# Optimization experiments

Measured on AMD Instinct MI355X. Metric: run time of the kernel, lower is better.

## Reference

```python
import jax, jax.numpy as jnp
import numpy as np
import math

V, BS, D, L, H = 50257, 1024, 768, 12, 4
DH = D // H  # 192
B, T = 4, 1024


def setup_inputs() -> dict:
    key = jax.random.key(0)
    ks = jax.random.split(key, 18)
    s = 0.02
    inp = {
        "x": jax.random.randint(ks[0], (B, T), 0, V),
        "tok_emb": jax.random.normal(ks[1], (V, D), jnp.float32) * s,
        "pos_emb": jax.random.normal(ks[2], (BS, D), jnp.float32) * s,
        "ln1_s": jnp.ones((L, D), jnp.float32),
        "ln1_b": jnp.zeros((L, D), jnp.float32),
        "qkv_w": jax.random.normal(ks[3], (L, D, 3 * D), jnp.float32) * s,
        "qkv_b": jnp.zeros((L, 3 * D), jnp.float32),
        "ln2_s": jnp.ones((L, D), jnp.float32),
        "ln2_b": jnp.zeros((L, D), jnp.float32),
        "fc_w": jax.random.normal(ks[4], (L, D, 4 * D), jnp.float32) * s,
        "fc_b": jnp.zeros((L, 4 * D), jnp.float32),
        "proj_w": jax.random.normal(ks[5], (L, 4 * D, D), jnp.float32) * s,
        "proj_b": jnp.zeros((L, D), jnp.float32),
        "lnf_s": jnp.ones((D,), jnp.float32),
        "lnf_b": jnp.zeros((D,), jnp.float32),
        "head_w": jax.random.normal(ks[6], (D, V), jnp.float32) * s,
        "head_b": jnp.zeros((V,), jnp.float32),
    }
    return inp


def _ln(x, scale, shift):
    m = x.mean(-1, keepdims=True)
    v = jnp.mean((x - m) ** 2, axis=-1, keepdims=True)
    return (x - m) * jax.lax.rsqrt(v + 1e-5) * scale + shift


def _forward(x, tok_emb, pos_emb, ln1_s, ln1_b, qkv_w, qkv_b, ln2_s, ln2_b,
             fc_w, fc_b, proj_w, proj_b, lnf_s, lnf_b, head_w, head_b):
    Bx, Tx = x.shape
    h = tok_emb[x] + pos_emb[:Tx]  # [B,T,D]
    causal = jnp.tril(jnp.ones((Tx, Tx), bool))
    scale = 1.0 / math.sqrt(DH)

    def block(h, p):
        s1, b1, wq, bq, s2, b2, wf, bf, wp, bp = p
        # attention (no output projection, faithful to source)
        ln1 = _ln(h, s1, b1)
        qkv = ln1 @ wq + bq  # [B,T,3D]
        q, k, v = jnp.split(qkv, 3, axis=-1)
        q = q.reshape(Bx, Tx, H, DH)
        k = k.reshape(Bx, Tx, H, DH)
        v = v.reshape(Bx, Tx, H, DH)
        att = jnp.einsum('bthd,bshd->bhts', q, k) * scale
        att = jnp.where(causal, att, -jnp.inf)
        att = jax.nn.softmax(att, axis=-1)
        y = jnp.einsum('bhts,bshd->bthd', att, v).reshape(Bx, Tx, D)
        h = h + y
        # MLP (ReLU, despite attr named gelu in source)
        ln2 = _ln(h, s2, b2)
        m = jax.nn.relu(ln2 @ wf + bf) @ wp + bp
        return h + m, None

    h, _ = jax.lax.scan(block, h,
                        (ln1_s, ln1_b, qkv_w, qkv_b, ln2_s, ln2_b,
                         fc_w, fc_b, proj_w, proj_b))
    h = _ln(h, lnf_s, lnf_b)
    return h @ head_w + head_b  # [B,T,V]


def reference(x, tok_emb, pos_emb, ln1_s, ln1_b, qkv_w, qkv_b, ln2_s, ln2_b,
              fc_w, fc_b, proj_w, proj_b, lnf_s, lnf_b, head_w, head_b):
    return _forward(x, tok_emb, pos_emb, ln1_s, ln1_b, qkv_w, qkv_b,
                    ln2_s, ln2_b, fc_w, fc_b, proj_w, proj_b,
                    lnf_s, lnf_b, head_w, head_b)
```

## Files before the change

kernel.cpp:

```cpp
#include <hip/hip_runtime.h>
#include <stdint.h>

#define D_MODEL 768
#define NHEAD 4
#define DHEAD 192
#define SEQ 1024
#define NLAYER 12
#define NTOK 4096
#define NVOCAB 50257

typedef __attribute__((ext_vector_type(4))) float f32x4;
typedef __attribute__((ext_vector_type(4))) int i32x4;
typedef __attribute__((ext_vector_type(4))) unsigned short u16x4;

__device__ __forceinline__ unsigned short f2bf(float f) {
  unsigned u = __builtin_bit_cast(unsigned, f);
  u += 0x7FFFu + ((u >> 16) & 1u);
  return (unsigned short)(u >> 16);
}

#define GLDS(src, dst)                                                   \
  __builtin_amdgcn_global_load_lds(                                      \
      (const __attribute__((address_space(1))) void*)(src),              \
      (__attribute__((address_space(3))) void*)(dst), 16, 0, 0)

#define FENCE asm volatile("" ::: "memory")
#define BAR()                         \
  do {                                \
    FENCE;                            \
    __builtin_amdgcn_s_barrier();     \
    FENCE;                            \
  } while (0)

__global__ __launch_bounds__(256) void embed_kernel(
    const int* __restrict__ x, const float* __restrict__ tok,
    const float* __restrict__ pos, float* __restrict__ h) {
  int row = blockIdx.x;
  int t = row & (SEQ - 1);
  int id = x[row];
  const float* tp = tok + (long)id * D_MODEL;
  const float* pp = pos + (long)t * D_MODEL;
  float* hp = h + (long)row * D_MODEL;
  for (int j = threadIdx.x; j < D_MODEL; j += 256)
    hp[j] = tp[j] + pp[j];
}

__global__ __launch_bounds__(256) void ln_kernel(
    const float* __restrict__ h, const float* __restrict__ sc,
    const float* __restrict__ sh, unsigned short* __restrict__ out) {
  __shared__ float red[4];
  int row = blockIdx.x;
  const float* x = h + (long)row * D_MODEL;
  int tid = threadIdx.x;
  float v0 = x[tid], v1 = x[tid + 256], v2 = x[tid + 512];
  float s = v0 + v1 + v2;
  for (int o = 32; o > 0; o >>= 1) s += __shfl_xor(s, o);
  if ((tid & 63) == 0) red[tid >> 6] = s;
  __syncthreads();
  float mean = (red[0] + red[1] + red[2] + red[3]) * (1.0f / D_MODEL);
  __syncthreads();
  float d0 = v0 - mean, d1 = v1 - mean, d2 = v2 - mean;
  float q = d0 * d0 + d1 * d1 + d2 * d2;
  for (int o = 32; o > 0; o >>= 1) q += __shfl_xor(q, o);
  if ((tid & 63) == 0) red[tid >> 6] = q;
  __syncthreads();
  float var = (red[0] + red[1] + red[2] + red[3]) * (1.0f / D_MODEL);
  float r = rsqrtf(var + 1e-5f);
  unsigned short* op = out + (long)row * D_MODEL;
  op[tid]       = f2bf(d0 * r * sc[tid]       + sh[tid]);
  op[tid + 256] = f2bf(d1 * r * sc[tid + 256] + sh[tid + 256]);
  op[tid + 512] = f2bf(d2 * r * sc[tid + 512] + sh[tid + 512]);
}

__global__ __launch_bounds__(256) void wtrans3_kernel(
    const float* __restrict__ qw, const float* __restrict__ fw,
    const float* __restrict__ pw, unsigned short* __restrict__ tq,
    unsigned short* __restrict__ tf, unsigned short* __restrict__ tp) {
  __shared__ unsigned short tile[32][33];
  int bid = blockIdx.x;
  const float* src; unsigned short* dst; int K, N, nb;
  if (bid < 1728)               { src = qw; dst = tq; K = 768;  N = 2304; nb = 72; }
  else if ((bid -= 1728) < 2304){ src = fw; dst = tf; K = 768;  N = 3072; nb = 96; }
  else { bid -= 2304;             src = pw; dst = tp; K = 3072; N = 768;  nb = 24; }
  int n0 = (bid % nb) * 32, k0 = (bid / nb) * 32;
  int tx = threadIdx.x & 31, ty = threadIdx.x >> 5;
  #pragma unroll
  for (int i = 0; i < 4; ++i) {
    int k = k0 + ty + i * 8;
    tile[ty + i * 8][tx] = f2bf(src[(long)k * N + n0 + tx]);
  }
  __syncthreads();
  #pragma unroll
  for (int i = 0; i < 4; ++i) {
    int nn = n0 + ty + i * 8;
    dst[(long)nn * K + k0 + tx] = tile[tx][ty + i * 8];
  }
}

__global__ __launch_bounds__(256) void wtrans_kernel(
    const float* __restrict__ w, unsigned short* __restrict__ wt, int K, int N) {
  __shared__ unsigned short tile[32][33];
  int n0 = blockIdx.x * 32, k0 = blockIdx.y * 32;
  int tx = threadIdx.x, ty = threadIdx.y;
  int n = n0 + tx; if (n >= N) n = N - 1;
  #pragma unroll
  for (int i = 0; i < 4; ++i) {
    int k = k0 + ty + i * 8;
    tile[ty + i * 8][tx] = f2bf(w[(long)k * N + n]);
  }
  __syncthreads();
  #pragma unroll
  for (int i = 0; i < 4; ++i) {
    int nn = n0 + ty + i * 8;
    if (nn < N) wt[(long)nn * K + k0 + tx] = tile[tx][ty + i * 8];
  }
}

__global__ __launch_bounds__(256) void vt_kernel(
    const unsigned short* __restrict__ qkv, unsigned short* __restrict__ vt) {
  __shared__ unsigned short tile[32][33];
  int bh = blockIdx.z, b = bh >> 2, hh = bh & 3;
  int t0 = blockIdx.x * 32, f0 = blockIdx.y * 32;
  int tx = threadIdx.x, ty = threadIdx.y;
  const unsigned short* src = qkv + (long)b * SEQ * 2304 + 2 * D_MODEL + hh * DHEAD;
  #pragma unroll
  for (int i = 0; i < 4; ++i) {
    int t = t0 + ty + i * 8;
    tile[ty + i * 8][tx] = src[(long)t * 2304 + f0 + tx];
  }
  __syncthreads();
  unsigned short* dst = vt + (long)bh * DHEAD * SEQ;
  #pragma unroll
  for (int i = 0; i < 4; ++i) {
    int f = f0 + ty + i * 8;
    dst[(long)f * SEQ + t0 + tx] = tile[tx][ty + i * 8];
  }
}

__global__ __launch_bounds__(256) void softmax_kernel(
    const float* __restrict__ S, unsigned short* __restrict__ P) {
  __shared__ float red[4];
  long rid = blockIdx.x;
  int q = (int)(rid & (SEQ - 1));
  int tid = threadIdx.x;
  int i0 = tid * 4;
  f32x4 v;
  if (i0 <= q) {
    v = *(const f32x4*)(S + rid * SEQ + i0);
  } else {
    v = f32x4{-3.0e38f, -3.0e38f, -3.0e38f, -3.0e38f};
  }
  float m = -3.0e38f;
  #pragma unroll
  for (int j = 0; j < 4; ++j) {
    if (i0 + j > q) v[j] = -3.0e38f;
    m = fmaxf(m, v[j]);
  }
  for (int o = 32; o > 0; o >>= 1) m = fmaxf(m, __shfl_xor(m, o));
  if ((tid & 63) == 0) red[tid >> 6] = m;
  __syncthreads();
  m = fmaxf(fmaxf(red[0], red[1]), fmaxf(red[2], red[3]));
  __syncthreads();
  float e[4];
  float sum = 0.f;
  #pragma unroll
  for (int j = 0; j < 4; ++j) {
    e[j] = (i0 + j > q) ? 0.f : __expf(v[j] - m);
    sum += e[j];
  }
  for (int o = 32; o > 0; o >>= 1) sum += __shfl_xor(sum, o);
  if ((tid & 63) == 0) red[tid >> 6] = sum;
  __syncthreads();
  float inv = 1.0f / (red[0] + red[1] + red[2] + red[3]);
  if ((i0 >> 7) <= (q >> 7)) {
    u16x4 out;
    #pragma unroll
    for (int j = 0; j < 4; ++j) out[j] = f2bf(e[j] * inv);
    *(u16x4*)(P + rid * SEQ + i0) = out;
  }
}

template<int MODE>
__global__ __launch_bounds__(512, 2) void gemm256_kernel(
    const unsigned short* __restrict__ A,
    const unsigned short* __restrict__ B,
    const float* __restrict__ bias,
    void* __restrict__ Cv, int ldc,
    int M, int N, int K, int mb) {
  __shared__ __align__(16) unsigned short lds[2][2][2][128 * 64];

  int tid = threadIdx.x;
  int lane = tid & 63;
  int wid = tid >> 6;
  int wm = wid >> 2;
  int wn = wid & 3;

  int bid = blockIdx.x;
  int mpx = mb >> 3;
  int xcd = bid & 7;
  int c = bid >> 3;
  int m0 = (xcd * mpx + (c & (mpx - 1))) * 256;
  int n0 = (c / mpx) * 256;

  auto stageA = [&](int buf, int half, int kt) {
    const unsigned short* src = A + (long)(m0 + half * 128) * K + kt * 64;
    #pragma unroll
    for (int i = 0; i < 2; ++i) {
      int chunk = i * 8 + wid;
      int r = chunk * 8 + (lane >> 3);
      int cc = ((lane & 7) ^ (lane >> 3)) << 3;
      GLDS(src + (long)r * K + cc, &lds[buf][0][half][chunk * 512]);
    }
  };
  auto stageB = [&](int buf, int half, int kt) {
    #pragma unroll
    for (int i = 0; i < 2; ++i) {
      int chunk = i * 8 + wid;
      int r = chunk * 8 + (lane >> 3);
      int cc = ((lane & 7) ^ (lane >> 3)) << 3;
      int rg = n0 + half * 128 + r;
      if (rg >= N) rg = N - 1;
      GLDS(B + (long)rg * K + kt * 64 + cc, &lds[buf][1][half][chunk * 512]);
    }
  };

  auto lda_frag = [&](int buf, int f, int s) -> i32x4 {
    int r = wm * 64 + (f & 3) * 16 + (lane & 15);
    int kb = s * 64 + ((lane >> 4) << 4);
    int off = r * 128 + (kb ^ ((r & 7) << 4));
    return *(const i32x4*)((const char*)&lds[buf][0][f >> 2][0] + off);
  };
  auto ldb_frag = [&](int buf, int gg, int s) -> i32x4 {
    int r = wn * 32 + (gg & 1) * 16 + (lane & 15);
    int kb = s * 64 + ((lane >> 4) << 4);
    int off = r * 128 + (kb ^ ((r & 7) << 4));
    return *(const i32x4*)((const char*)&lds[buf][1][gg >> 1][0] + off);
  };

  f32x4 acc[8][4] = {};
  i32x4 a[4][2], b[4][2];

  int nt = K / 64;

  stageA(0, 0, 0); stageB(0, 0, 0); stageB(0, 1, 0); stageA(0, 1, 0);
  stageA(1, 0, 1); stageB(1, 0, 1); stageB(1, 1, 1);
  asm volatile("s_waitcnt vmcnt(6)" ::: "memory");
  BAR();

  for (int t = 0; t < nt; ++t) {
    int buf = t & 1, nbuf = buf ^ 1;
    #pragma unroll
    for (int fi = 0; fi < 4; ++fi) {
      a[fi][0] = lda_frag(buf, fi, 0);
      a[fi][1] = lda_frag(buf, fi, 1);
    }
    #pragma unroll
    for (int gi = 0; gi < 2; ++gi) {
      b[gi][0] = ldb_frag(buf, gi, 0);
      b[gi][1] = ldb_frag(buf, gi, 1);
    }
    if (t + 1 < nt) stageA(nbuf, 1, t + 1);
    BAR();
    __builtin_amdgcn_s_setprio(1);
    #pragma unroll
    for (int s = 0; s < 2; ++s)
      #pragma unroll
      for (int fi = 0; fi < 4; ++fi)
        #pragma unroll
        for (int gi = 0; gi < 2; ++gi)
          asm("v_mfma_f32_16x16x32_bf16 %0, %1, %2, %0"
              : "+v"(acc[fi][gi]) : "v"(b[gi][s]), "v"(a[fi][s]));
    __builtin_amdgcn_s_setprio(0);
    BAR();
    #pragma unroll
    for (int gi = 2; gi < 4; ++gi) {
      b[gi][0] = ldb_frag(buf, gi, 0);
      b[gi][1] = ldb_frag(buf, gi, 1);
    }
    if (t + 2 < nt) stageA(buf, 0, t + 2);
    BAR();
    __builtin_amdgcn_s_setprio(1);
    #pragma unroll
    for (int s = 0; s < 2; ++s)
      #pragma unroll
      for (int fi = 0; fi < 4; ++fi)
        #pragma unroll
        for (int gi = 2; gi < 4; ++gi)
          asm("v_mfma_f32_16x16x32_bf16 %0, %1, %2, %0"
              : "+v"(acc[fi][gi]) : "v"(b[gi][s]), "v"(a[fi][s]));
    __builtin_amdgcn_s_setprio(0);
    BAR();
    #pragma unroll
    for (int fi = 0; fi < 4; ++fi) {
      a[fi][0] = lda_frag(buf, 4 + fi, 0);
      a[fi][1] = lda_frag(buf, 4 + fi, 1);
    }
    if (t + 2 < nt) stageB(buf, 0, t + 2);
    BAR();
    __builtin_amdgcn_s_setprio(1);
    #pragma unroll
    for (int s = 0; s < 2; ++s)
      #pragma unroll
      for (int fi = 0; fi < 4; ++fi)
        #pragma unroll
        for (int gi = 2; gi < 4; ++gi)
          asm("v_mfma_f32_16x16x32_bf16 %0, %1, %2, %0"
              : "+v"(acc[4 + fi][gi]) : "v"(b[gi][s]), "v"(a[fi][s]));
    __builtin_amdgcn_s_setprio(0);
    BAR();
    if (t + 2 < nt) {
      stageB(buf, 1, t + 2);
      asm volatile("s_waitcnt vmcnt(6)" ::: "memory");
    } else if (t + 1 < nt) {
      asm volatile("s_waitcnt vmcnt(0)" ::: "memory");
    }
    BAR();
    __builtin_amdgcn_s_setprio(1);
    #pragma unroll
    for (int s = 0; s < 2; ++s)
      #pragma unroll
      for (int fi = 0; fi < 4; ++fi)
        #pragma unroll
        for (int gi = 0; gi < 2; ++gi)
          asm("v_mfma_f32_16x16x32_bf16 %0, %1, %2, %0"
              : "+v"(acc[4 + fi][gi]) : "v"(b[gi][s]), "v"(a[fi][s]));
    __builtin_amdgcn_s_setprio(0);
    BAR();
  }

  int cr = lane & 15;
  int cg = (lane >> 4) << 2;
  #pragma unroll
  for (int f = 0; f < 8; ++f) {
    long row = m0 + wm * 64 + (f & 3) * 16 + (f >> 2) * 128 + cr;
    #pragma unroll
    for (int gg = 0; gg < 4; ++gg) {
      int col = n0 + wn * 32 + (gg & 1) * 16 + (gg >> 1) * 128 + cg;
      f32x4 v = acc[f][gg];
      if (MODE == 0 || MODE == 1) {
        f32x4 bv = *(const f32x4*)(bias + col);
        u16x4 o;
        #pragma unroll
        for (int r = 0; r < 4; ++r) {
          float tt = v[r] + bv[r];
          if (MODE == 1) tt = fmaxf(tt, 0.f);
          o[r] = f2bf(tt);
        }
        *(u16x4*)((unsigned short*)Cv + row * (long)ldc + col) = o;
      } else {
        float* cp = (float*)Cv + row * (long)ldc + col;
        if (col + 4 <= N) {
          f32x4 bv = *(const f32x4*)(bias + col);
          f32x4 o;
          #pragma unroll
          for (int r = 0; r < 4; ++r) o[r] = v[r] + bv[r];
          *(f32x4*)cp = o;
        } else {
          #pragma unroll
          for (int r = 0; r < 4; ++r)
            if (col + r < N) cp[r] = v[r] + bias[col + r];
        }
      }
    }
  }
}

#define BM 128
#define BN 128
#define BKK 32

template<int MODE>
__global__ __launch_bounds__(256) void gemm_kernel(
    const unsigned short* __restrict__ A, int lda,
    const unsigned short* __restrict__ B, int ldb,
    const float* __restrict__ bias,
    void* __restrict__ Cv, int ldc,
    int M, int N, int K,
    int NI, long sAo, long sAi, long sBo, long sBi,
    long sCo, long sCi, float alpha, int causal, int mblocks) {
  __shared__ __align__(16) unsigned short As[2][BM * BKK];
  __shared__ __align__(16) unsigned short Bs[2][BN * BKK];
  int z = blockIdx.z;
  int zo = z / NI, zi = z - zo * NI;
  A += zo * sAo + zi * sAi;
  B += zo * sBo + zi * sBi;
  long coff = zo * sCo + zi * sCi;

  int m0, n0;
  if (mblocks > 0) {
    int bid = blockIdx.x;
    int mpx = mblocks >> 3;
    int xcd = bid & 7;
    int c = bid >> 3;
    m0 = (xcd * mpx + (c & (mpx - 1))) * BM;
    n0 = (c / mpx) * BN;
  } else {
    m0 = blockIdx.y * BM;
    n0 = blockIdx.x * BN;
  }
  if (causal == 1 && n0 > m0 + BM - 1) return;
  int kmax = (causal == 2) ? min(K, m0 + BM) : K;

  int tid = threadIdx.x;
  int lane = tid & 63;
  int wave = tid >> 6;
  int wm = (wave >> 1) * 64;
  int wn = (wave & 1) * 64;

  auto stage = [&](int buf, int k0) {
    #pragma unroll
    for (int i = 0; i < 2; ++i) {
      int c0 = i * 256 + wave * 64;
      int cc = c0 + lane;
      int row = cc >> 2;
      int ko = (cc & 3) << 3;
      GLDS(A + (long)(m0 + row) * lda + k0 + ko, As[buf] + c0 * 8);
      int rg = n0 + row; if (rg >= N) rg = N - 1;
      GLDS(B + (long)rg * ldb + k0 + ko, Bs[buf] + c0 * 8);
    }
  };

  f32x4 acc[4][4] = {};
  int nt = kmax / BKK;
  stage(0, 0);
  __syncthreads();
  int cur = 0;
  for (int t = 0; t < nt; ++t) {
    if (t + 1 < nt) stage(cur ^ 1, (t + 1) * BKK);
    int lr = lane & 15;
    int kg = (lane >> 4) << 3;
    i32x4 af[4], bf[4];
    #pragma unroll
    for (int mi = 0; mi < 4; ++mi)
      af[mi] = *(const i32x4*)(As[cur] + (wm + mi * 16 + lr) * BKK + kg);
    #pragma unroll
    for (int ni = 0; ni < 4; ++ni)
      bf[ni] = *(const i32x4*)(Bs[cur] + (wn + ni * 16 + lr) * BKK + kg);
    #pragma unroll
    for (int mi = 0; mi < 4; ++mi)
      #pragma unroll
      for (int ni = 0; ni < 4; ++ni)
        asm("v_mfma_f32_16x16x32_bf16 %0, %1, %2, %0"
            : "+v"(acc[mi][ni]) : "v"(bf[ni]), "v"(af[mi]));
    __syncthreads();
    cur ^= 1;
  }

  int cm = lane & 15;
  int cg = (lane >> 4) << 2;
  #pragma unroll
  for (int mi = 0; mi < 4; ++mi) {
    long row = m0 + wm + mi * 16 + cm;
    #pragma unroll
    for (int ni = 0; ni < 4; ++ni) {
      int col = n0 + wn + ni * 16 + cg;
      f32x4 v = acc[mi][ni];
      if (MODE == 2) {
        #pragma unroll
        for (int r = 0; r < 4; ++r) v[r] *= alpha;
        *(f32x4*)((float*)Cv + coff + row * (long)ldc + col) = v;
      } else if (MODE == 0 || MODE == 1) {
        f32x4 bv = *(const f32x4*)(bias + col);
        u16x4 o;
        #pragma unroll
        for (int r = 0; r < 4; ++r) {
          float t = v[r] + bv[r];
          if (MODE == 1) t = fmaxf(t, 0.f);
          o[r] = f2bf(t);
        }
        *(u16x4*)((unsigned short*)Cv + coff + row * (long)ldc + col) = o;
      } else {
        float* cp = (float*)Cv + coff + row * (long)ldc + col;
        if (col + 4 <= N) {
          f32x4 bv = bias ? *(const f32x4*)(bias + col)
                          : f32x4{0.f, 0.f, 0.f, 0.f};
          if (MODE == 3) {
            f32x4 old = *(f32x4*)cp;
            #pragma unroll
            for (int r = 0; r < 4; ++r) old[r] += v[r] + bv[r];
            *(f32x4*)cp = old;
          } else {
            f32x4 o;
            #pragma unroll
            for (int r = 0; r < 4; ++r) o[r] = v[r] + bv[r];
            *(f32x4*)cp = o;
          }
        } else {
          #pragma unroll
          for (int r = 0; r < 4; ++r) {
            if (col + r < N) {
              float bvr = bias ? bias[col + r] : 0.f;
              if (MODE == 3) cp[r] += v[r] + bvr;
              else           cp[r] = v[r] + bvr;
            }
          }
        }
      }
    }
  }
}

extern "C" void kernel_launch(void* const* d_in, const int* in_sizes, int n_in,
                              void* d_out, int out_size, void* d_ws, size_t ws_size,
                              hipStream_t stream) {
  const int*   x       = (const int*)  d_in[0];
  const float* tok_emb = (const float*)d_in[1];
  const float* pos_emb = (const float*)d_in[2];
  const float* ln1_s   = (const float*)d_in[3];
  const float* ln1_b   = (const float*)d_in[4];
  const float* qkv_w   = (const float*)d_in[5];
  const float* qkv_b   = (const float*)d_in[6];
  const float* ln2_s   = (const float*)d_in[7];
  const float* ln2_b   = (const float*)d_in[8];
  const float* fc_w    = (const float*)d_in[9];
  const float* fc_b    = (const float*)d_in[10];
  const float* proj_w  = (const float*)d_in[11];
  const float* proj_b  = (const float*)d_in[12];
  const float* lnf_s   = (const float*)d_in[13];
  const float* lnf_b   = (const float*)d_in[14];
  const float* head_w  = (const float*)d_in[15];
  const float* head_b  = (const float*)d_in[16];

  char* ws = (char*)d_ws;
  size_t off = 0;
  auto alloc = [&](size_t bytes) {
    char* p = ws + off;
    off += (bytes + 255) & ~(size_t)255;
    return p;
  };
  float*          h   = (float*)         alloc((size_t)NTOK * D_MODEL * 4);
  unsigned short* lnb = (unsigned short*)alloc((size_t)NTOK * D_MODEL * 2);
  unsigned short* qkv = (unsigned short*)alloc((size_t)NTOK * 2304 * 2);
  unsigned short* vt  = (unsigned short*)alloc((size_t)16 * DHEAD * SEQ * 2);
  unsigned short* mid = (unsigned short*)alloc((size_t)NTOK * 3072 * 2);
  float*          S   = (float*)         alloc((size_t)16 * SEQ * SEQ * 4);
  unsigned short* P   = (unsigned short*)alloc((size_t)16 * SEQ * SEQ * 2);
  unsigned short* wtq = (unsigned short*)alloc((size_t)2304 * 768 * 2);
  unsigned short* wtf = (unsigned short*)alloc((size_t)3072 * 768 * 2);
  unsigned short* wtp = (unsigned short*)alloc((size_t)768 * 3072 * 2);
  unsigned short* wth = (unsigned short*)alloc((size_t)50304 * 768 * 2);

  embed_kernel<<<NTOK, 256, 0, stream>>>(x, tok_emb, pos_emb, h);

  const float rscale = 0.07216878364870323f;

  for (int l = 0; l < NLAYER; ++l) {
    wtrans3_kernel<<<6336, 256, 0, stream>>>(
        qkv_w + (long)l * 768 * 2304, fc_w + (long)l * 768 * 3072,
        proj_w + (long)l * 3072 * 768, wtq, wtf, wtp);
    ln_kernel<<<NTOK, 256, 0, stream>>>(h, ln1_s + l * 768, ln1_b + l * 768, lnb);
    gemm256_kernel<0><<<16 * 9, 512, 0, stream>>>(
        lnb, wtq, qkv_b + l * 2304, qkv, 2304, 4096, 2304, 768, 16);
    vt_kernel<<<dim3(32, 6, 16), dim3(32, 8), 0, stream>>>(qkv, vt);
    gemm_kernel<2><<<dim3(8, 8, 16), 256, 0, stream>>>(
        qkv, 2304, qkv + 768, 2304, nullptr, S, 1024,
        1024, 1024, 192, 4,
        (long)1024 * 2304, 192, (long)1024 * 2304, 192,
        (long)4 * 1024 * 1024, (long)1024 * 1024, rscale, 1, 0);
    softmax_kernel<<<16384, 256, 0, stream>>>(S, P);
    gemm_kernel<3><<<dim3(2, 8, 16), 256, 0, stream>>>(
        P, 1024, vt, 1024, nullptr, h, 768,
        1024, 192, 1024, 4,
        (long)4 * 1024 * 1024, (long)1024 * 1024,
        (long)4 * 192 * 1024, (long)192 * 1024,
        (long)1024 * 768, 192, 1.0f, 2, 0);
    ln_kernel<<<NTOK, 256, 0, stream>>>(h, ln2_s + l * 768, ln2_b + l * 768, lnb);
    gemm256_kernel<1><<<16 * 12, 512, 0, stream>>>(
        lnb, wtf, fc_b + l * 3072, mid, 3072, 4096, 3072, 768, 16);
    gemm_kernel<3><<<192, 256, 0, stream>>>(
        mid, 3072, wtp, 3072, proj_b + l * 768, h, 768,
        4096, 768, 3072, 1, 0, 0, 0, 0, 0, 0, 1.0f, 0, 32);
  }

  wtrans_kernel<<<dim3(1571, 24), dim3(32, 8), 0, stream>>>(head_w, wth, 768, 50257);
  ln_kernel<<<NTOK, 256, 0, stream>>>(h, lnf_s, lnf_b, lnb);
  gemm256_kernel<4><<<16 * 197, 512, 0, stream>>>(
      lnb, wth, head_b, (float*)d_out, 50257, 4096, 50257, 768, 16);
}
```

Baseline: 3.181 ms.

## Replace QK^T GEMM with causal-aware MFMA kernel skipping masked tiles

Replaces the generic tiled GEMM for attention scores with a dedicated kernel in which each block handles 16 query rows and computes only the 16-wide key tiles at or below the diagonal. Q fragments stay in registers and K fragments are loaded directly from global memory without LDS staging. Blocks are ordered to interleave long and short rows for load balance. This roughly halves the QK^T FLOPs, but K is reloaded from global/L2 by every block with no shared-memory reuse, and the upper-triangle of S is left unwritten, relying on softmax masking.

```diff
diff --git a/kernel.cpp b/kernel.cpp
--- a/kernel.cpp
+++ b/kernel.cpp
@@ -134,6 +134,43 @@
   for (int i = 0; i < 4; ++i) {
     int f = f0 + ty + i * 8;
     dst[(long)f * SEQ + t0 + tx] = tile[tx][ty + i * 8];
+  }
+}
+
+__global__ __launch_bounds__(256) void qk_kernel(
+    const unsigned short* __restrict__ qkv, float* __restrict__ S) {
+  const float rscale = 0.07216878364870323f;
+  int tid = threadIdx.x;
+  int lane = tid & 63, wid = tid >> 6;
+  int l15 = lane & 15, g = lane >> 4;
+  int bid = blockIdx.x;
+  int bh = bid & 15;
+  int p = bid >> 4;
+  int qt = (p & 1) ? (p >> 1) : (63 - (p >> 1));
+  int b = bh >> 2, hh = bh & 3;
+  const unsigned short* Qb = qkv + ((long)b * 1024 + qt * 16) * 2304 + hh * 192;
+  const unsigned short* Kb = qkv + (long)b * 1024 * 2304 + 768 + hh * 192;
+  float* Srow = S + ((long)bh * 1024 + qt * 16) * 1024;
+
+  i32x4 qfr[6];
+  #pragma unroll
+  for (int kb = 0; kb < 6; ++kb)
+    qfr[kb] = *(const i32x4*)(Qb + (long)l15 * 2304 + kb * 32 + g * 8);
+
+  int nsf = qt + 1;
+  for (int sf = wid; sf < nsf; sf += 4) {
+    f32x4 sacc = {};
+    #pragma unroll
+    for (int kb = 0; kb < 6; ++kb) {
+      i32x4 kf = *(const i32x4*)(Kb + (long)(sf * 16 + l15) * 2304 + kb * 32 + g * 8);
+      asm("v_mfma_f32_16x16x32_bf16 %0, %1, %2, %0"
+          : "+v"(sacc) : "v"(kf), "v"(qfr[kb]));
+    }
+    asm volatile("s_nop 7\n\ts_nop 7\n\ts_nop 7" : "+v"(sacc));
+    f32x4 st;
+    #pragma unroll
+    for (int e = 0; e < 4; ++e) st[e] = sacc[e] * rscale;
+    *(f32x4*)(Srow + (long)l15 * 1024 + sf * 16 + 4 * g) = st;
   }
 }
 
@@ -542,8 +579,6 @@
 
   embed_kernel<<<NTOK, 256, 0, stream>>>(x, tok_emb, pos_emb, h);
 
-  const float rscale = 0.07216878364870323f;
-
   for (int l = 0; l < NLAYER; ++l) {
     wtrans3_kernel<<<6336, 256, 0, stream>>>(
         qkv_w + (long)l * 768 * 2304, fc_w + (long)l * 768 * 3072,
@@ -552,11 +587,7 @@
     gemm256_kernel<0><<<16 * 9, 512, 0, stream>>>(
         lnb, wtq, qkv_b + l * 2304, qkv, 2304, 4096, 2304, 768, 16);
     vt_kernel<<<dim3(32, 6, 16), dim3(32, 8), 0, stream>>>(qkv, vt);
-    gemm_kernel<2><<<dim3(8, 8, 16), 256, 0, stream>>>(
-        qkv, 2304, qkv + 768, 2304, nullptr, S, 1024,
-        1024, 1024, 192, 4,
-        (long)1024 * 2304, 192, (long)1024 * 2304, 192,
-        (long)4 * 1024 * 1024, (long)1024 * 1024, rscale, 1, 0);
+    qk_kernel<<<1024, 256, 0, stream>>>(qkv, S);
     softmax_kernel<<<16384, 256, 0, stream>>>(S, P);
     gemm_kernel<3><<<dim3(2, 8, 16), 256, 0, stream>>>(
         P, 1024, vt, 1024, nullptr, h, 768,
```

Measured after the change: 3.427 ms. +7.7%, slower.

## Add K=32 double-buffered 256x256 GEMM with launch bounds 2 for LM head

Applied to the files above, without the earlier changes.

Adds a new 256x256-tile bf16 MFMA GEMM that stages K in 32-wide slices into a smaller double-buffered LDS footprint. Loads of the next slices are interleaved between four MFMA sub-phases, with XOR-swizzled LDS addressing and raised wave priority around the MFMAs. The kernel requests two blocks per CU through its launch bounds. It is used only for the final vocabulary projection, aiming to improve occupancy and overlap of global loads with compute on the largest GEMM. In exchange it adds more barriers per K step and more register pressure.

```diff
diff --git a/kernel.cpp b/kernel.cpp
--- a/kernel.cpp
+++ b/kernel.cpp
@@ -360,6 +360,152 @@
           for (int r = 0; r < 4; ++r)
             if (col + r < N) cp[r] = v[r] + bias[col + r];
         }
+      }
+    }
+  }
+}
+
+__global__ __launch_bounds__(512, 2) void gemm256k32_kernel(
+    const unsigned short* __restrict__ A,
+    const unsigned short* __restrict__ B,
+    const float* __restrict__ bias,
+    float* __restrict__ C, int ldc,
+    int M, int N, int K, int mb) {
+  __shared__ __align__(16) unsigned short lds[2][2][2][128 * 32];
+
+  int tid = threadIdx.x;
+  int lane = tid & 63;
+  int wid = tid >> 6;
+  int wm = wid >> 2;
+  int wn = wid & 3;
+
+  int bid = blockIdx.x;
+  int mpx = mb >> 3;
+  int xcd = bid & 7;
+  int c = bid >> 3;
+  int m0 = (xcd * mpx + (c & (mpx - 1))) * 256;
+  int n0 = (c / mpx) * 256;
+
+  auto stageA = [&](int buf, int half, int kt) {
+    const unsigned short* src = A + (long)(m0 + half * 128) * K + kt * 32;
+    int chunk = wid * 64 + lane;
+    int r = chunk >> 2;
+    int ce = (((chunk & 3) ^ (r & 3)) << 3);
+    GLDS(src + (long)r * K + ce, &lds[buf][0][half][chunk * 8]);
+  };
+  auto stageB = [&](int buf, int half, int kt) {
+    int chunk = wid * 64 + lane;
+    int r = chunk >> 2;
+    int ce = (((chunk & 3) ^ (r & 3)) << 3);
+    int rg = n0 + half * 128 + r;
+    if (rg >= N) rg = N - 1;
+    GLDS(B + (long)rg * K + kt * 32 + ce, &lds[buf][1][half][chunk * 8]);
+  };
+
+  auto lda_frag = [&](int buf, int f) -> i32x4 {
+    int r = wm * 64 + (f & 3) * 16 + (lane & 15);
+    int kb = (lane >> 4) << 4;
+    int off = r * 64 + (kb ^ ((r & 3) << 4));
+    return *(const i32x4*)((const char*)&lds[buf][0][f >> 2][0] + off);
+  };
+  auto ldb_frag = [&](int buf, int gg) -> i32x4 {
+    int r = wn * 32 + (gg & 1) * 16 + (lane & 15);
+    int kb = (lane >> 4) << 4;
+    int off = r * 64 + (kb ^ ((r & 3) << 4));
+    return *(const i32x4*)((const char*)&lds[buf][1][gg >> 1][0] + off);
+  };
+
+  f32x4 acc[8][4] = {};
+  i32x4 a[4], b[4];
+
+  int nt = K / 32;
+
+  stageA(0, 0, 0); stageB(0, 0, 0); stageB(0, 1, 0); stageA(0, 1, 0);
+  stageA(1, 0, 1); stageB(1, 0, 1); stageB(1, 1, 1);
+  asm volatile("s_waitcnt vmcnt(3)" ::: "memory");
+  BAR();
+
+  for (int t = 0; t < nt; ++t) {
+    int buf = t & 1, nbuf = buf ^ 1;
+    #pragma unroll
+    for (int fi = 0; fi < 4; ++fi) a[fi] = lda_frag(buf, fi);
+    #pragma unroll
+    for (int gi = 0; gi < 2; ++gi) b[gi] = ldb_frag(buf, gi);
+    if (t + 1 < nt) stageA(nbuf, 1, t + 1);
+    BAR();
+    __builtin_amdgcn_s_setprio(1);
+    #pragma unroll
+    for (int fi = 0; fi < 4; ++fi)
+      #pragma unroll
+      for (int gi = 0; gi < 2; ++gi)
+        asm("v_mfma_f32_16x16x32_bf16 %0, %1, %2, %0"
+            : "+v"(acc[fi][gi]) : "v"(b[gi]), "v"(a[fi]));
+    __builtin_amdgcn_s_setprio(0);
+    BAR();
+    #pragma unroll
+    for (int gi = 2; gi < 4; ++gi) b[gi] = ldb_frag(buf, gi);
+    if (t + 2 < nt) stageA(buf, 0, t + 2);
+    BAR();
+    __builtin_amdgcn_s_setprio(1);
+    #pragma unroll
+    for (int fi = 0; fi < 4; ++fi)
+      #pragma unroll
+      for (int gi = 2; gi < 4; ++gi)
+        asm("v_mfma_f32_16x16x32_bf16 %0, %1, %2, %0"
+            : "+v"(acc[fi][gi]) : "v"(b[gi]), "v"(a[fi]));
+    __builtin_amdgcn_s_setprio(0);
+    BAR();
+    #pragma unroll
+    for (int fi = 0; fi < 4; ++fi) a[fi] = lda_frag(buf, 4 + fi);
+    if (t + 2 < nt) stageB(buf, 0, t + 2);
+    BAR();
+    __builtin_amdgcn_s_setprio(1);
+    #pragma unroll
+    for (int fi = 0; fi < 4; ++fi)
+      #pragma unroll
+      for (int gi = 2; gi < 4; ++gi)
+        asm("v_mfma_f32_16x16x32_bf16 %0, %1, %2, %0"
+            : "+v"(acc[4 + fi][gi]) : "v"(b[gi]), "v"(a[fi]));
+    __builtin_amdgcn_s_setprio(0);
+    BAR();
+    if (t + 2 < nt) {
+      stageB(buf, 1, t + 2);
+      asm volatile("s_waitcnt vmcnt(3)" ::: "memory");
+    } else if (t + 1 < nt) {
+      asm volatile("s_waitcnt vmcnt(0)" ::: "memory");
+    }
+    BAR();
+    __builtin_amdgcn_s_setprio(1);
+    #pragma unroll
+    for (int fi = 0; fi < 4; ++fi)
+      #pragma unroll
+      for (int gi = 0; gi < 2; ++gi)
+        asm("v_mfma_f32_16x16x32_bf16 %0, %1, %2, %0"
+            : "+v"(acc[4 + fi][gi]) : "v"(b[gi]), "v"(a[fi]));
+    __builtin_amdgcn_s_setprio(0);
+    BAR();
+  }
+
+  int cr = lane & 15;
+  int cg = (lane >> 4) << 2;
+  #pragma unroll
+  for (int f = 0; f < 8; ++f) {
+    long row = m0 + wm * 64 + (f & 3) * 16 + (f >> 2) * 128 + cr;
+    #pragma unroll
+    for (int gg = 0; gg < 4; ++gg) {
+      int col = n0 + wn * 32 + (gg & 1) * 16 + (gg >> 1) * 128 + cg;
+      f32x4 v = acc[f][gg];
+      float* cp = C + row * (long)ldc + col;
+      if (col + 4 <= N) {
+        f32x4 bv = *(const f32x4*)(bias + col);
+        f32x4 o;
+        #pragma unroll
+        for (int r = 0; r < 4; ++r) o[r] = v[r] + bv[r];
+        *(f32x4*)cp = o;
+      } else {
+        #pragma unroll
+        for (int r = 0; r < 4; ++r)
+          if (col + r < N) cp[r] = v[r] + bias[col + r];
       }
     }
   }
@@ -574,6 +720,6 @@
 
   wtrans_kernel<<<dim3(1571, 24), dim3(32, 8), 0, stream>>>(head_w, wth, 768, 50257);
   ln_kernel<<<NTOK, 256, 0, stream>>>(h, lnf_s, lnf_b, lnb);
-  gemm256_kernel<4><<<16 * 197, 512, 0, stream>>>(
+  gemm256k32_kernel<<<16 * 197, 512, 0, stream>>>(
       lnb, wth, head_b, (float*)d_out, 50257, 4096, 50257, 768, 16);
 }
```

New measurement: 3.221 ms. No clear change (+1.3%).

## Fuse causal softmax into QK^T and PV GEMM epilogues with atomic row sums

Applied to the files above, without the earlier changes.

Removes the standalone softmax kernel and the fp32 score buffer. The QK^T GEMM epilogue now applies the causal mask and writes exp(scaled score) directly as bf16 probabilities, accumulating per-row sums with atomics. The PV GEMM epilogue divides by the row sum before adding into the residual. This avoids writing and re-reading a large fp32 score matrix each layer, but it drops the max subtraction, so it relies on attention scores staying small enough not to overflow exp. It also adds atomic contention on the row-sum buffer.

```diff
diff --git a/kernel.cpp b/kernel.cpp
--- a/kernel.cpp
+++ b/kernel.cpp
@@ -134,49 +134,6 @@
   for (int i = 0; i < 4; ++i) {
     int f = f0 + ty + i * 8;
     dst[(long)f * SEQ + t0 + tx] = tile[tx][ty + i * 8];
-  }
-}
-
-__global__ __launch_bounds__(256) void softmax_kernel(
-    const float* __restrict__ S, unsigned short* __restrict__ P) {
-  __shared__ float red[4];
-  long rid = blockIdx.x;
-  int q = (int)(rid & (SEQ - 1));
-  int tid = threadIdx.x;
-  int i0 = tid * 4;
-  f32x4 v;
-  if (i0 <= q) {
-    v = *(const f32x4*)(S + rid * SEQ + i0);
-  } else {
-    v = f32x4{-3.0e38f, -3.0e38f, -3.0e38f, -3.0e38f};
-  }
-  float m = -3.0e38f;
-  #pragma unroll
-  for (int j = 0; j < 4; ++j) {
-    if (i0 + j > q) v[j] = -3.0e38f;
-    m = fmaxf(m, v[j]);
-  }
-  for (int o = 32; o > 0; o >>= 1) m = fmaxf(m, __shfl_xor(m, o));
-  if ((tid & 63) == 0) red[tid >> 6] = m;
-  __syncthreads();
-  m = fmaxf(fmaxf(red[0], red[1]), fmaxf(red[2], red[3]));
-  __syncthreads();
-  float e[4];
-  float sum = 0.f;
-  #pragma unroll
-  for (int j = 0; j < 4; ++j) {
-    e[j] = (i0 + j > q) ? 0.f : __expf(v[j] - m);
-    sum += e[j];
-  }
-  for (int o = 32; o > 0; o >>= 1) sum += __shfl_xor(sum, o);
-  if ((tid & 63) == 0) red[tid >> 6] = sum;
-  __syncthreads();
-  float inv = 1.0f / (red[0] + red[1] + red[2] + red[3]);
-  if ((i0 >> 7) <= (q >> 7)) {
-    u16x4 out;
-    #pragma unroll
-    for (int j = 0; j < 4; ++j) out[j] = f2bf(e[j] * inv);
-    *(u16x4*)(P + rid * SEQ + i0) = out;
   }
 }
 
@@ -377,7 +334,8 @@
     void* __restrict__ Cv, int ldc,
     int M, int N, int K,
     int NI, long sAo, long sAi, long sBo, long sBi,
-    long sCo, long sCi, float alpha, int causal, int mblocks) {
+    long sCo, long sCi, float alpha, int causal, int mblocks,
+    float* __restrict__ rowsum) {
   __shared__ __align__(16) unsigned short As[2][BM * BKK];
   __shared__ __align__(16) unsigned short Bs[2][BN * BKK];
   int z = blockIdx.z;
@@ -451,52 +409,55 @@
   #pragma unroll
   for (int mi = 0; mi < 4; ++mi) {
     long row = m0 + wm + mi * 16 + cm;
+    float rs = 0.f;
     #pragma unroll
     for (int ni = 0; ni < 4; ++ni) {
       int col = n0 + wn + ni * 16 + cg;
       f32x4 v = acc[mi][ni];
-      if (MODE == 2) {
-        #pragma unroll
-        for (int r = 0; r < 4; ++r) v[r] *= alpha;
-        *(f32x4*)((float*)Cv + coff + row * (long)ldc + col) = v;
-      } else if (MODE == 0 || MODE == 1) {
-        f32x4 bv = *(const f32x4*)(bias + col);
+      if (MODE == 6) {
         u16x4 o;
         #pragma unroll
         for (int r = 0; r < 4; ++r) {
-          float t = v[r] + bv[r];
-          if (MODE == 1) t = fmaxf(t, 0.f);
-          o[r] = f2bf(t);
+          float e = (col + r <= (int)row) ? __expf(v[r] * alpha) : 0.f;
+          rs += e;
+          o[r] = f2bf(e);
         }
         *(u16x4*)((unsigned short*)Cv + coff + row * (long)ldc + col) = o;
+      } else if (MODE == 7) {
+        float inv = 1.0f / rowsum[(long)blockIdx.z * SEQ + row];
+        float* cp = (float*)Cv + coff + row * (long)ldc + col;
+        if (col + 4 <= N) {
+          f32x4 old = *(f32x4*)cp;
+          #pragma unroll
+          for (int r = 0; r < 4; ++r) old[r] += v[r] * inv;
+          *(f32x4*)cp = old;
+        } else {
+          #pragma unroll
+          for (int r = 0; r < 4; ++r)
+            if (col + r < N) cp[r] += v[r] * inv;
+        }
       } else {
         float* cp = (float*)Cv + coff + row * (long)ldc + col;
         if (col + 4 <= N) {
           f32x4 bv = bias ? *(const f32x4*)(bias + col)
                           : f32x4{0.f, 0.f, 0.f, 0.f};
-          if (MODE == 3) {
-            f32x4 old = *(f32x4*)cp;
-            #pragma unroll
-            for (int r = 0; r < 4; ++r) old[r] += v[r] + bv[r];
-            *(f32x4*)cp = old;
-          } else {
-            f32x4 o;
-            #pragma unroll
-            for (int r = 0; r < 4; ++r) o[r] = v[r] + bv[r];
-            *(f32x4*)cp = o;
-          }
+          f32x4 old = *(f32x4*)cp;
+          #pragma unroll
+          for (int r = 0; r < 4; ++r) old[r] += v[r] + bv[r];
+          *(f32x4*)cp = old;
         } else {
           #pragma unroll
           for (int r = 0; r < 4; ++r) {
             if (col + r < N) {
               float bvr = bias ? bias[col + r] : 0.f;
-              if (MODE == 3) cp[r] += v[r] + bvr;
-              else           cp[r] = v[r] + bvr;
+              cp[r] += v[r] + bvr;
             }
           }
         }
       }
     }
+    if (MODE == 6)
+      atomicAdd(rowsum + (long)blockIdx.z * SEQ + row, rs);
   }
 }
 
@@ -533,18 +494,21 @@
   unsigned short* qkv = (unsigned short*)alloc((size_t)NTOK * 2304 * 2);
   unsigned short* vt  = (unsigned short*)alloc((size_t)16 * DHEAD * SEQ * 2);
   unsigned short* mid = (unsigned short*)alloc((size_t)NTOK * 3072 * 2);
-  float*          S   = (float*)         alloc((size_t)16 * SEQ * SEQ * 4);
   unsigned short* P   = (unsigned short*)alloc((size_t)16 * SEQ * SEQ * 2);
+  float*          rsm = (float*)         alloc((size_t)NLAYER * 16 * SEQ * 4);
   unsigned short* wtq = (unsigned short*)alloc((size_t)2304 * 768 * 2);
   unsigned short* wtf = (unsigned short*)alloc((size_t)3072 * 768 * 2);
   unsigned short* wtp = (unsigned short*)alloc((size_t)768 * 3072 * 2);
   unsigned short* wth = (unsigned short*)alloc((size_t)50304 * 768 * 2);
 
+  hipMemsetAsync(rsm, 0, (size_t)NLAYER * 16 * SEQ * 4, stream);
+
   embed_kernel<<<NTOK, 256, 0, stream>>>(x, tok_emb, pos_emb, h);
 
   const float rscale = 0.07216878364870323f;
 
   for (int l = 0; l < NLAYER; ++l) {
+    float* rowsum = rsm + (long)l * 16 * SEQ;
     wtrans3_kernel<<<6336, 256, 0, stream>>>(
         qkv_w + (long)l * 768 * 2304, fc_w + (long)l * 768 * 3072,
         proj_w + (long)l * 3072 * 768, wtq, wtf, wtp);
@@ -552,24 +516,23 @@
     gemm256_kernel<0><<<16 * 9, 512, 0, stream>>>(
         lnb, wtq, qkv_b + l * 2304, qkv, 2304, 4096, 2304, 768, 16);
     vt_kernel<<<dim3(32, 6, 16), dim3(32, 8), 0, stream>>>(qkv, vt);
-    gemm_kernel<2><<<dim3(8, 8, 16), 256, 0, stream>>>(
-        qkv, 2304, qkv + 768, 2304, nullptr, S, 1024,
+    gemm_kernel<6><<<dim3(8, 8, 16), 256, 0, stream>>>(
+        qkv, 2304, qkv + 768, 2304, nullptr, P, 1024,
         1024, 1024, 192, 4,
         (long)1024 * 2304, 192, (long)1024 * 2304, 192,
-        (long)4 * 1024 * 1024, (long)1024 * 1024, rscale, 1, 0);
-    softmax_kernel<<<16384, 256, 0, stream>>>(S, P);
-    gemm_kernel<3><<<dim3(2, 8, 16), 256, 0, stream>>>(
+        (long)4 * 1024 * 1024, (long)1024 * 1024, rscale, 1, 0, rowsum);
+    gemm_kernel<7><<<dim3(2, 8, 16), 256, 0, stream>>>(
         P, 1024, vt, 1024, nullptr, h, 768,
         1024, 192, 1024, 4,
         (long)4 * 1024 * 1024, (long)1024 * 1024,
         (long)4 * 192 * 1024, (long)192 * 1024,
-        (long)1024 * 768, 192, 1.0f, 2, 0);
+        (long)1024 * 768, 192, 1.0f, 2, 0, rowsum);
     ln_kernel<<<NTOK, 256, 0, stream>>>(h, ln2_s + l * 768, ln2_b + l * 768, lnb);
     gemm256_kernel<1><<<16 * 12, 512, 0, stream>>>(
         lnb, wtf, fc_b + l * 3072, mid, 3072, 4096, 3072, 768, 16);
     gemm_kernel<3><<<192, 256, 0, stream>>>(
         mid, 3072, wtp, 3072, proj_b + l * 768, h, 768,
-        4096, 768, 3072, 1, 0, 0, 0, 0, 0, 0, 1.0f, 0, 32);
+        4096, 768, 3072, 1, 0, 0, 0, 0, 0, 0, 1.0f, 0, 32, nullptr);
   }
 
   wtrans_kernel<<<dim3(1571, 24), dim3(32, 8), 0, stream>>>(head_w, wth, 768, 50257);
```

Measured after the change: 3.121 ms. About the same (-1.9%).
